# Optimization experiments

Measured on AMD Instinct MI355X. Metric: run time of the kernel, lower is better.

## Reference

```python
import jax, jax.numpy as jnp
import numpy as np

H = 128  # hidden/input size fixed by module


def setup_inputs() -> dict:
    key = jax.random.key(0)
    ks = jax.random.split(key, 8)
    S, B = 512, 256
    scale = 1.0 / np.sqrt(H)
    return {
        "X": jax.random.normal(ks[0], (S, B, H), dtype=jnp.float32),
        "h": jax.random.normal(ks[1], (1, B, H), dtype=jnp.float32),
        "lin_W": jax.random.uniform(ks[2], (H, H), jnp.float32, -scale, scale),
        "lin_b": jax.random.uniform(ks[3], (H,), jnp.float32, -scale, scale),
        "W_ih": jax.random.uniform(ks[4], (3 * H, H), jnp.float32, -scale, scale),
        "W_hh": jax.random.uniform(ks[5], (3 * H, H), jnp.float32, -scale, scale),
        "b_ih": jax.random.uniform(ks[6], (3 * H,), jnp.float32, -scale, scale),
        "b_hh": jax.random.uniform(ks[7], (3 * H,), jnp.float32, -scale, scale),
    }


def reference(X, h, lin_W, lin_b, W_ih, W_hh, b_ih, b_hh):
    # Linear: y = X @ W^T + b   (torch nn.Linear convention)
    Xp = jnp.einsum("sbd,ed->sbe", X, lin_W) + lin_b
    # Precompute input-hidden gate projections for all timesteps: (S, B, 3H)
    gx_all = jnp.einsum("sbd,gd->sbg", Xp, W_ih) + b_ih

    def step(h_t, gx):
        gh = h_t @ W_hh.T + b_hh  # (B, 3H)
        xr, xz, xn = jnp.split(gx, 3, axis=-1)
        hr, hz, hn = jnp.split(gh, 3, axis=-1)
        r = jax.nn.sigmoid(xr + hr)
        z = jax.nn.sigmoid(xz + hz)
        n = jnp.tanh(xn + r * hn)
        h_new = (1.0 - z) * n + z * h_t
        return h_new, h_new

    _, outs = jax.lax.scan(step, h[0], gx_all)
    return outs  # (S, B, H) — the module returns only the output sequence
```

## Files before the change

### kernel.cpp

```cpp
#include <hip/hip_runtime.h>
#include <math.h>

#define HID 128
#define G3  384
#define BATCH 256
#define SEQ 512
#define NB 16
#define NBLK (BATCH/NB)
#define NB2 2
#define NBLK2 (BATCH/NB2)
#define GHP 392

typedef __bf16 bf16x8 __attribute__((ext_vector_type(8)));
typedef __bf16 bf16x4 __attribute__((ext_vector_type(4)));
typedef float  f32x4  __attribute__((ext_vector_type(4)));

#define LOG2E 1.44269504088896f
#define SC_RZ (-1.44269504088896f)
#define SC_N  (-2.88539008177793f)

__device__ __forceinline__ float sigm(float x) {
    return __builtin_amdgcn_rcpf(1.f + __builtin_amdgcn_exp2f(-LOG2E * x));
}
__device__ __forceinline__ float tanh_fast(float x) {
    float e = __builtin_amdgcn_exp2f(-2.f * LOG2E * x);
    return __builtin_amdgcn_rcpf(1.f + e) * 2.f - 1.f;
}
__device__ __forceinline__ f32x4 mfma16(bf16x8 a, bf16x8 b, f32x4 c) {
    return __builtin_amdgcn_mfma_f32_16x16x32_bf16(a, b, c, 0, 0, 0);
}
__device__ __forceinline__ bf16x8 cvt8(float4 a, float4 b) {
    bf16x8 f;
    f[0] = (__bf16)a.x; f[1] = (__bf16)a.y; f[2] = (__bf16)a.z; f[3] = (__bf16)a.w;
    f[4] = (__bf16)b.x; f[5] = (__bf16)b.y; f[6] = (__bf16)b.z; f[7] = (__bf16)b.w;
    return f;
}
__device__ __forceinline__ bf16x8 cvt8s(float4 a, float4 b, float s) {
    bf16x8 f;
    f[0] = (__bf16)(a.x*s); f[1] = (__bf16)(a.y*s); f[2] = (__bf16)(a.z*s); f[3] = (__bf16)(a.w*s);
    f[4] = (__bf16)(b.x*s); f[5] = (__bf16)(b.y*s); f[6] = (__bf16)(b.z*s); f[7] = (__bf16)(b.w*s);
    return f;
}
__device__ __forceinline__ bf16x4 cvt4(float4 a) {
    bf16x4 f;
    f[0] = (__bf16)a.x; f[1] = (__bf16)a.y; f[2] = (__bf16)a.z; f[3] = (__bf16)a.w;
    return f;
}


__global__ void fold_bf16_kernel(const float* __restrict__ lin_W,
                                 const float* __restrict__ lin_b,
                                 const float* __restrict__ W_ih,
                                 const float* __restrict__ b_ih,
                                 __bf16* __restrict__ Wcbf,
                                 float* __restrict__ bcA) {
    const int g = blockIdx.x;
    const int d = threadIdx.x;
    const float sc = (g < 2 * HID) ? SC_RZ : SC_N;
    float acc = 0.f;
    #pragma unroll 16
    for (int e = 0; e < HID; ++e) acc += W_ih[g * HID + e] * lin_W[e * HID + d];
    Wcbf[g * HID + d] = (__bf16)(acc * sc);
    if (d == 0) {
        float b = 0.f;
        for (int e = 0; e < HID; ++e) b += W_ih[g * HID + e] * lin_b[e];
        bcA[g] = (b + b_ih[g]) * sc;
    }
}

#define GEMM_TILE(MT, CUR, NXT)                                               \
  {                                                                           \
    int mtn_ = (MT) + 1; if (mtn_ > 7) mtn_ = 7;                              \
    const float* pxn_ = X + (size_t)(m0 + mtn_ * 16 + col) * HID + lr * 8;    \
    _Pragma("unroll")                                                         \
    for (int kt = 0; kt < 4; ++kt) {                                          \
        NXT[2 * kt]     = *(const float4*)(pxn_ + kt * 32);                   \
        NXT[2 * kt + 1] = *(const float4*)(pxn_ + kt * 32 + 4);               \
    }                                                                         \
    bf16x8 Bx_[4];                                                            \
    _Pragma("unroll")                                                         \
    for (int kt = 0; kt < 4; ++kt) Bx_[kt] = cvt8(CUR[2 * kt], CUR[2 * kt + 1]); \
    const int m_ = m0 + (MT) * 16 + col;                                      \
    _Pragma("unroll")                                                         \
    for (int j = 0; j < 6; ++j) {                                             \
        f32x4 acc_ = vb[j];                                                   \
        acc_ = mfma16(A[j][0], Bx_[0], acc_);                                 \
        acc_ = mfma16(A[j][1], Bx_[1], acc_);                                 \
        acc_ = mfma16(A[j][2], Bx_[2], acc_);                                 \
        acc_ = mfma16(A[j][3], Bx_[3], acc_);                                 \
        float4 o_; o_.x = acc_[0]; o_.y = acc_[1]; o_.z = acc_[2]; o_.w = acc_[3]; \
        *(bf16x4*)(gx + (size_t)m_ * G3 + (w * 6 + j) * 16 + lr * 4) = cvt4(o_); \
    }                                                                         \
  }

__global__ __launch_bounds__(256, 2)
void gemm_gx2(const float* __restrict__ X,
              const __bf16* __restrict__ Wcbf,
              const float* __restrict__ bcA,
              __bf16* __restrict__ gx) {
    const int t   = threadIdx.x;
    const int w   = t >> 6;
    const int l   = t & 63;
    const int col = l & 15;
    const int lr  = l >> 4;
    const int m0  = blockIdx.x * 128;

    bf16x8 A[6][4];
    #pragma unroll
    for (int j = 0; j < 6; ++j)
        #pragma unroll
        for (int kt = 0; kt < 4; ++kt)
            A[j][kt] = *(const bf16x8*)(Wcbf +
                (size_t)((w * 6 + j) * 16 + col) * HID + kt * 32 + lr * 8);
    #pragma unroll
    for (int j = 0; j < 6; ++j)
        #pragma unroll
        for (int kt = 0; kt < 4; ++kt)
            asm volatile("" : "+v"(A[j][kt]));

    f32x4 vb[6];
    #pragma unroll
    for (int j = 0; j < 6; ++j)
        vb[j] = *(const f32x4*)(bcA + (w * 6 + j) * 16 + lr * 4);

    float4 xe[8], xo[8];
    {
        const float* px = X + (size_t)(m0 + col) * HID + lr * 8;
        #pragma unroll
        for (int kt = 0; kt < 4; ++kt) {
            xe[2 * kt]     = *(const float4*)(px + kt * 32);
            xe[2 * kt + 1] = *(const float4*)(px + kt * 32 + 4);
        }
    }
    for (int mt = 0; mt < 8; mt += 2) {
        GEMM_TILE(mt,     xe, xo);
        GEMM_TILE(mt + 1, xo, xe);
    }
}

#define SPLIT_STEP(S, C0, C1, C2, N0, N1, N2)                                 \
  {                                                                           \
               \
    bf16x8 Bh_[4];                                                            \
    _Pragma("unroll")                                                         \
    for (int kt = 0; kt < 4; ++kt)                                            \
        Bh_[kt] = *(const bf16x8*)(hbuf + SW(col, kt * 64 + lr * 16));        \
    f32x4 ar_ = vbr, az_ = vbz, anh_ = vbnh;                                  \
    _Pragma("unroll")                                                         \
    for (int kt = 0; kt < 4; ++kt) {                                          \
        ar_  = mfma16(aW[0][kt], Bh_[kt], ar_);                               \
        az_  = mfma16(aW[1][kt], Bh_[kt], az_);                               \
        anh_ = mfma16(aW[2][kt], Bh_[kt], anh_);                              \
    }                                                                         \
    if (col < NB2) {                                                          \
        float* gp_ = ghsF + col * GHP + w * 16 + lr * 4;                      \
        *(f32x4*)(gp_)       = ar_;                                           \
        *(f32x4*)(gp_ + 128) = az_;                                           \
        *(f32x4*)(gp_ + 256) = anh_;                                          \
    }                                                                         \
    asm volatile("s_waitcnt lgkmcnt(0)" ::: "memory");                        \
    __builtin_amdgcn_s_barrier();                                             \
                           \
    if (t < 256) {                                                            \
        int sp_ = (S) + 1; if (sp_ > SEQ - 1) sp_ = SEQ - 1;                  \
        const __bf16* p_ = gx + (size_t)sp_ * (BATCH * G3) + gxoff;           \
        asm volatile("global_load_ushort %0, %3, off\n\t"                     \
                     "global_load_ushort %1, %3, off offset:256\n\t"          \
                     "global_load_ushort %2, %3, off offset:512"              \
                     : "=&v"(N0), "=&v"(N1), "=&v"(N2) : "v"(p_) : "memory"); \
        float gr_ = ghsF[bi * GHP + ri];                                      \
        float gz_ = ghsF[bi * GHP + 128 + ri];                                \
        float gn_ = ghsF[bi * GHP + 256 + ri];                                \
          \
        asm volatile("s_waitcnt vmcnt(4)" ::: "memory");                      \
        __builtin_amdgcn_sched_barrier(0);                                    \
        float xr_ = __uint_as_float((C0) << 16);                              \
        float xz_ = __uint_as_float((C1) << 16);                              \
        float xn_ = __uint_as_float((C2) << 16);                              \
        float r_ = __builtin_amdgcn_rcpf(1.f + __builtin_amdgcn_exp2f(gr_ + xr_)); \
        float z_ = __builtin_amdgcn_rcpf(1.f + __builtin_amdgcn_exp2f(gz_ + xz_)); \
        float n_ = 2.f * __builtin_amdgcn_rcpf(1.f + __builtin_amdgcn_exp2f(xn_ + r_ * gn_)) - 1.f; \
        float hn_ = n_ + z_ * (hold - n_);                                    \
        hold = hn_;                                                           \
        *(__bf16*)(hbuf + SW(bi, ri * 2)) = (__bf16)hn_;                      \
        out[((size_t)(S) * BATCH + bb + bi) * HID + ri] = hn_;                \
    }                                                                         \
    asm volatile("s_waitcnt lgkmcnt(0)" ::: "memory");                        \
    __builtin_amdgcn_s_barrier();                                             \
  }

__global__ __launch_bounds__(512, 2)
void gru_scan_split2(const float* __restrict__ h0,
                     const float* __restrict__ W_hh,
                     const float* __restrict__ b_hh,
                     const __bf16* __restrict__ gx,
                     float* __restrict__ out) {
    const int t   = threadIdx.x;
    const int w   = t >> 6;
    const int l   = t & 63;
    const int col = l & 15;
    const int lr  = l >> 4;
    const int bb  = blockIdx.x * NB2;
    const int bi  = t >> 7;
    const int ri  = t & 127;

    __shared__ __align__(16) unsigned char lds[4096 + NB2 * GHP * 4];
    unsigned char* hbuf = lds;
    float* ghsF = (float*)(lds + 4096);

    auto SW = [](int b, int off) { return b * 256 + (off ^ ((b & 7) << 4)); };

    bf16x8 aW[3][4];
    #pragma unroll
    for (int g3 = 0; g3 < 3; ++g3) {
        const float s = (g3 < 2) ? SC_RZ : SC_N;
        #pragma unroll
        for (int kt = 0; kt < 4; ++kt) {
            const int row = g3 * HID + w * 16 + col;
            const float* pw = W_hh + row * HID + kt * 32 + lr * 8;
            aW[g3][kt] = cvt8s(*(const float4*)pw, *(const float4*)(pw + 4), s);
        }
    }
    #pragma unroll
    for (int g3 = 0; g3 < 3; ++g3)
        #pragma unroll
        for (int kt = 0; kt < 4; ++kt)
            asm volatile("" : "+v"(aW[g3][kt]));

    f32x4 vbr, vbz, vbnh;
    #pragma unroll
    for (int q = 0; q < 4; ++q) {
        const int g = w * 16 + lr * 4 + q;
        vbr[q]  = b_hh[g] * SC_RZ;
        vbz[q]  = b_hh[HID + g] * SC_RZ;
        vbnh[q] = b_hh[2 * HID + g] * SC_N;
    }

    float hold = 0.f;
    if (t < 256) hold = h0[(size_t)(bb + bi) * HID + ri];
    asm volatile("" :: "v"(hold), "v"(vbr), "v"(vbz), "v"(vbnh));

    const size_t gxoff = (size_t)(bb + bi) * G3 + ri;

    if (t < 32) {
        const int sb = t >> 4, k8 = (t & 15) * 8;
        const float* ph = h0 + (size_t)(bb + sb) * HID + k8;
        *(bf16x8*)(hbuf + SW(sb, k8 * 2)) =
            cvt8(*(const float4*)ph, *(const float4*)(ph + 4));
    } else if (t < 256) {
        const int sb = t >> 4, k8 = (t & 15) * 8;
        uint4 z = {0u, 0u, 0u, 0u};
        *(uint4*)(hbuf + SW(sb, k8 * 2)) = z;
    }

    unsigned c0 = 0, c1 = 0, c2 = 0, n0, n1, n2, dm;
    if (t < 256) {
        const __bf16* p_ = gx + gxoff;
        asm volatile("global_load_ushort %0, %3, off\n\t"
                     "global_load_ushort %1, %3, off offset:256\n\t"
                     "global_load_ushort %2, %3, off offset:512"
                     : "=&v"(c0), "=&v"(c1), "=&v"(c2) : "v"(p_) : "memory");
        asm volatile("global_load_ushort %0, %1, off"
                     : "=&v"(dm) : "v"(p_) : "memory");
    }
    asm volatile("s_waitcnt lgkmcnt(0)" ::: "memory");
    __builtin_amdgcn_s_barrier();

    for (int s0 = 0; s0 < SEQ; s0 += 2) {
        SPLIT_STEP(s0,     c0, c1, c2, n0, n1, n2);
        SPLIT_STEP(s0 + 1, n0, n1, n2, c0, c1, c2);
    }
    if (t < 256) asm volatile("" :: "v"(dm));
}

__global__ void fold_kernel(const float* __restrict__ lin_W,
                            const float* __restrict__ lin_b,
                            const float* __restrict__ W_ih,
                            const float* __restrict__ b_ih,
                            float* __restrict__ Wc,
                            float* __restrict__ bcA) {
    const int g = blockIdx.x;
    const int d = threadIdx.x;
    float acc = 0.f;
    for (int e = 0; e < HID; ++e) acc += W_ih[g * HID + e] * lin_W[e * HID + d];
    Wc[g * HID + d] = acc;
    if (d == 0) {
        float b = 0.f;
        for (int e = 0; e < HID; ++e) b += W_ih[g * HID + e] * lin_b[e];
        bcA[g] = b + b_ih[g];
    }
}

__global__ __launch_bounds__(512, 2)
void gru_scan_mfma(const float* __restrict__ X,
                   const float* __restrict__ h0,
                   const float* __restrict__ W_hh,
                   const float* __restrict__ b_hh,
                   const float* __restrict__ Wc,
                   const float* __restrict__ bcA,
                   float* __restrict__ out) {
    const int t   = threadIdx.x;
    const int w   = t >> 6;
    const int l   = t & 63;
    const int col = l & 15;
    const int lr  = l >> 4;
    const int bb  = blockIdx.x * NB;

    __shared__ __align__(16) unsigned char lds[16384];
    unsigned char* hA = lds;
    unsigned char* hB = lds + 4096;
    unsigned char* xA = lds + 8192;
    unsigned char* xB = lds + 12288;

    auto SW = [](int b, int off) { return b * 256 + (off ^ ((b & 7) << 4)); };

    bf16x8 aW[3][4], aC[3][4];
    #pragma unroll
    for (int g3 = 0; g3 < 3; ++g3)
        #pragma unroll
        for (int kt = 0; kt < 4; ++kt) {
            const int row = g3 * HID + w * 16 + col;
            const float* pw = W_hh + row * HID + kt * 32 + lr * 8;
            const float* pc = Wc   + row * HID + kt * 32 + lr * 8;
            aW[g3][kt] = cvt8(*(const float4*)pw, *(const float4*)(pw + 4));
            aC[g3][kt] = cvt8(*(const float4*)pc, *(const float4*)(pc + 4));
        }
    #pragma unroll
    for (int g3 = 0; g3 < 3; ++g3)
        #pragma unroll
        for (int kt = 0; kt < 4; ++kt) {
            asm volatile("" : "+v"(aW[g3][kt]));
            asm volatile("" : "+v"(aC[g3][kt]));
        }

    f32x4 vbr, vbz, vbnx, vbnh;
    #pragma unroll
    for (int q = 0; q < 4; ++q) {
        const int g = w * 16 + lr * 4 + q;
        vbr[q]  = bcA[g] + b_hh[g];
        vbz[q]  = bcA[HID + g] + b_hh[HID + g];
        vbnx[q] = bcA[2 * HID + g];
        vbnh[q] = b_hh[2 * HID + g];
    }

    f32x4 hold = *(const f32x4*)(h0 + (size_t)(bb + col) * HID + w * 16 + lr * 4);

    const int sb = t >> 5;
    const int sk = (t & 31) * 4;

    float4 xp, xq;
    if (t < 256) {
        const int hb = t >> 4, hk = (t & 15) * 8;
        const float* ph = h0 + (size_t)(bb + hb) * HID + hk;
        *(bf16x8*)(hA + SW(hb, hk * 2)) =
            cvt8(*(const float4*)ph, *(const float4*)(ph + 4));
    }
    {
        const float* px = X + ((size_t)0 * BATCH + bb + sb) * HID + sk;
        *(bf16x4*)(xA + SW(sb, sk * 2)) = cvt4(*(const float4*)px);
        const float* p1 = X + ((size_t)1 * BATCH + bb + sb) * HID + sk;
        xp = *(const float4*)p1;
    }
    asm volatile("s_waitcnt lgkmcnt(0)" ::: "memory");
    __builtin_amdgcn_s_barrier();

    auto STEP = [&](int s, unsigned char* hR, unsigned char* hW,
                    unsigned char* xR, unsigned char* xW,
                    float4& xc, float4& xn) {
        *(bf16x4*)(xW + SW(sb, sk * 2)) = cvt4(xc);
        {
            int sp = s + 2; if (sp > SEQ - 1) sp = SEQ - 1;
            const float* px = X + ((size_t)sp * BATCH + bb + sb) * HID + sk;
            xn = *(const float4*)px;
        }
        bf16x8 Bh[4], Bx[4];
        #pragma unroll
        for (int kt = 0; kt < 4; ++kt) {
            Bh[kt] = *(const bf16x8*)(hR + SW(col, kt * 64 + lr * 16));
            Bx[kt] = *(const bf16x8*)(xR + SW(col, kt * 64 + lr * 16));
        }
        f32x4 ar = vbr, az = vbz, anh = vbnh, anx = vbnx;
        #pragma unroll
        for (int kt = 0; kt < 4; ++kt) {
            ar  = mfma16(aW[0][kt], Bh[kt], ar);
            ar  = mfma16(aC[0][kt], Bx[kt], ar);
            az  = mfma16(aW[1][kt], Bh[kt], az);
            az  = mfma16(aC[1][kt], Bx[kt], az);
            anh = mfma16(aW[2][kt], Bh[kt], anh);
            anx = mfma16(aC[2][kt], Bx[kt], anx);
        }
        f32x4 hnew;
        #pragma unroll
        for (int q = 0; q < 4; ++q) {
            float r = sigm(ar[q]);
            float z = sigm(az[q]);
            float n = tanh_fast(anx[q] + r * anh[q]);
            hnew[q] = n + z * (hold[q] - n);
        }
        hold = hnew;
        *(bf16x4*)(hW + SW(col, (w * 16 + lr * 4) * 2)) = cvt4(*(float4*)&hnew);
        float4 o; o.x = hnew[0]; o.y = hnew[1]; o.z = hnew[2]; o.w = hnew[3];
        *(float4*)(out + ((size_t)s * BATCH + bb + col) * HID + w * 16 + lr * 4) = o;
        asm volatile("s_waitcnt lgkmcnt(0)" ::: "memory");
        __builtin_amdgcn_s_barrier();
    };

    for (int s0 = 0; s0 < SEQ; s0 += 2) {
        STEP(s0,     hA, hB, xA, xB, xp, xq);
        STEP(s0 + 1, hB, hA, xB, xA, xq, xp);
    }
}

extern "C" void kernel_launch(void* const* d_in, const int* in_sizes, int n_in,
                              void* d_out, int out_size, void* d_ws, size_t ws_size,
                              hipStream_t stream) {
    const float* X     = (const float*)d_in[0];
    const float* h0    = (const float*)d_in[1];
    const float* lin_W = (const float*)d_in[2];
    const float* lin_b = (const float*)d_in[3];
    const float* W_ih  = (const float*)d_in[4];
    const float* W_hh  = (const float*)d_in[5];
    const float* b_ih  = (const float*)d_in[6];
    const float* b_hh  = (const float*)d_in[7];
    float* out = (float*)d_out;

    const size_t GX_BYTES   = (size_t)SEQ * BATCH * G3 * 2;
    const size_t WCBF_BYTES = (size_t)G3 * HID * 2;
    const size_t BCA_BYTES  = (size_t)G3 * 4;

    if (ws_size >= GX_BYTES + WCBF_BYTES + BCA_BYTES) {
        __bf16* gxp  = (__bf16*)d_ws;
        __bf16* Wcbf = (__bf16*)((char*)d_ws + GX_BYTES);
        float*  bcA  = (float*)((char*)d_ws + GX_BYTES + WCBF_BYTES);

        fold_bf16_kernel<<<G3, HID, 0, stream>>>(lin_W, lin_b, W_ih, b_ih, Wcbf, bcA);
        gemm_gx2<<<(SEQ * BATCH) / 128, 256, 0, stream>>>(X, Wcbf, bcA, gxp);
        gru_scan_split2<<<NBLK2, 512, 0, stream>>>(h0, W_hh, b_hh, gxp, out);
    } else {
        float* Wc  = (float*)d_ws;
        float* bcA = Wc + G3 * HID;
        fold_kernel<<<G3, HID, 0, stream>>>(lin_W, lin_b, W_ih, b_ih, Wc, bcA);
        gru_scan_mfma<<<NBLK, 512, 0, stream>>>(X, h0, W_hh, b_hh, Wc, bcA, out);
    }
}
```

Before: 354.3 us.

## Fuse input-projection GEMM into scan kernel with per-timestep-group readiness counters

```diff
diff --git a/kernel.cpp b/kernel.cpp
--- a/kernel.cpp
+++ b/kernel.cpp
@@ -7,8 +7,9 @@
 #define SEQ 512
 #define NB 16
 #define NBLK (BATCH/NB)
-#define NB2 2
-#define NBLK2 (BATCH/NB2)
+#define NBS 2
+#define NBLKS (BATCH/NBS)
+#define NGEMM 1024
 #define GHP 392
 
 typedef __bf16 bf16x8 __attribute__((ext_vector_type(8)));
@@ -68,10 +69,11 @@
     }
 }
 
-#define GEMM_TILE(MT, CUR, NXT)                                               \
+
+#define GEMM_TILE4(MT, CUR, NXT)                                              \
   {                                                                           \
-    int mtn_ = (MT) + 1; if (mtn_ > 7) mtn_ = 7;                              \
-    const float* pxn_ = X + (size_t)(m0 + mtn_ * 16 + col) * HID + lr * 8;    \
+    int mtn_ = (MT) + 1; if (mtn_ > 3) mtn_ = 3;                              \
+    const float* pxn_ = X + (size_t)(m0h + mtn_ * 16 + col) * HID + lr * 8;   \
     _Pragma("unroll")                                                         \
     for (int kt = 0; kt < 4; ++kt) {                                          \
         NXT[2 * kt]     = *(const float4*)(pxn_ + kt * 32);                   \
@@ -80,7 +82,7 @@
     bf16x8 Bx_[4];                                                            \
     _Pragma("unroll")                                                         \
     for (int kt = 0; kt < 4; ++kt) Bx_[kt] = cvt8(CUR[2 * kt], CUR[2 * kt + 1]); \
-    const int m_ = m0 + (MT) * 16 + col;                                      \
+    const int m_ = m0h + (MT) * 16 + col;                                     \
     _Pragma("unroll")                                                         \
     for (int j = 0; j < 6; ++j) {                                             \
         f32x4 acc_ = vb[j];                                                   \
@@ -89,54 +91,9 @@
         acc_ = mfma16(A[j][2], Bx_[2], acc_);                                 \
         acc_ = mfma16(A[j][3], Bx_[3], acc_);                                 \
         float4 o_; o_.x = acc_[0]; o_.y = acc_[1]; o_.z = acc_[2]; o_.w = acc_[3]; \
-        *(bf16x4*)(gx + (size_t)m_ * G3 + (w * 6 + j) * 16 + lr * 4) = cvt4(o_); \
+        *(bf16x4*)(gx + (size_t)m_ * G3 + (w4 * 6 + j) * 16 + lr * 4) = cvt4(o_); \
     }                                                                         \
   }
-
-__global__ __launch_bounds__(256, 2)
-void gemm_gx2(const float* __restrict__ X,
-              const __bf16* __restrict__ Wcbf,
-              const float* __restrict__ bcA,
-              __bf16* __restrict__ gx) {
-    const int t   = threadIdx.x;
-    const int w   = t >> 6;
-    const int l   = t & 63;
-    const int col = l & 15;
-    const int lr  = l >> 4;
-    const int m0  = blockIdx.x * 128;
-
-    bf16x8 A[6][4];
-    #pragma unroll
-    for (int j = 0; j < 6; ++j)
-        #pragma unroll
-        for (int kt = 0; kt < 4; ++kt)
-            A[j][kt] = *(const bf16x8*)(Wcbf +
-                (size_t)((w * 6 + j) * 16 + col) * HID + kt * 32 + lr * 8);
-    #pragma unroll
-    for (int j = 0; j < 6; ++j)
-        #pragma unroll
-        for (int kt = 0; kt < 4; ++kt)
-            asm volatile("" : "+v"(A[j][kt]));
-
-    f32x4 vb[6];
-    #pragma unroll
-    for (int j = 0; j < 6; ++j)
-        vb[j] = *(const f32x4*)(bcA + (w * 6 + j) * 16 + lr * 4);
-
-    float4 xe[8], xo[8];
-    {
-        const float* px = X + (size_t)(m0 + col) * HID + lr * 8;
-        #pragma unroll
-        for (int kt = 0; kt < 4; ++kt) {
-            xe[2 * kt]     = *(const float4*)(px + kt * 32);
-            xe[2 * kt + 1] = *(const float4*)(px + kt * 32 + 4);
-        }
-    }
-    for (int mt = 0; mt < 8; mt += 2) {
-        GEMM_TILE(mt,     xe, xo);
-        GEMM_TILE(mt + 1, xo, xe);
-    }
-}
 
 #define SPLIT_STEP(S, C0, C1, C2, N0, N1, N2)                                 \
   {                                                                           \
@@ -152,7 +109,7 @@
         az_  = mfma16(aW[1][kt], Bh_[kt], az_);                               \
         anh_ = mfma16(aW[2][kt], Bh_[kt], anh_);                              \
     }                                                                         \
-    if (col < NB2) {                                                          \
+    if (col < NBS) {                                                          \
         float* gp_ = ghsF + col * GHP + w * 16 + lr * 4;                      \
         *(f32x4*)(gp_)       = ar_;                                           \
         *(f32x4*)(gp_ + 128) = az_;                                           \
@@ -163,6 +120,15 @@
                            \
     if (t < 256) {                                                            \
         int sp_ = (S) + 1; if (sp_ > SEQ - 1) sp_ = SEQ - 1;                  \
+                               \
+        int g_ = sp_ >> 3;                                                    \
+        if (g_ != curgrp) {                                                   \
+            curgrp = g_;                                                      \
+            while (__hip_atomic_load(cnt + g_, __ATOMIC_RELAXED,              \
+                                     __HIP_MEMORY_SCOPE_AGENT) < 16u)         \
+                __builtin_amdgcn_s_sleep(2);                                  \
+            __threadfence();                                                  \
+        }                                                                     \
         const __bf16* p_ = gx + (size_t)sp_ * (BATCH * G3) + gxoff;           \
         asm volatile("global_load_ushort %0, %3, off\n\t"                     \
                      "global_load_ushort %1, %3, off offset:256\n\t"          \
@@ -171,7 +137,6 @@
         float gr_ = ghsF[bi * GHP + ri];                                      \
         float gz_ = ghsF[bi * GHP + 128 + ri];                                \
         float gn_ = ghsF[bi * GHP + 256 + ri];                                \
-          \
         asm volatile("s_waitcnt vmcnt(4)" ::: "memory");                      \
         __builtin_amdgcn_sched_barrier(0);                                    \
         float xr_ = __uint_as_float((C0) << 16);                              \
@@ -190,21 +155,75 @@
   }
 
 __global__ __launch_bounds__(512, 2)
-void gru_scan_split2(const float* __restrict__ h0,
+void fused_gemm_scan(const float* __restrict__ X,
+                     const __bf16* __restrict__ Wcbf,
+                     const float* __restrict__ bcA,
+                     __bf16* __restrict__ gx,
+                     unsigned* __restrict__ cnt,
+                     const float* __restrict__ h0,
                      const float* __restrict__ W_hh,
                      const float* __restrict__ b_hh,
-                     const __bf16* __restrict__ gx,
                      float* __restrict__ out) {
-    const int t   = threadIdx.x;
+    const int t = threadIdx.x;
+
+    if (blockIdx.x >= NBLKS) {
+        const int chunk = blockIdx.x - NBLKS;
+        const int wg  = t >> 8;
+        const int w4  = (t >> 6) & 3;
+        const int l   = t & 63;
+        const int col = l & 15;
+        const int lr  = l >> 4;
+        const int m0h = chunk * 128 + wg * 64;
+
+        bf16x8 A[6][4];
+        #pragma unroll
+        for (int j = 0; j < 6; ++j)
+            #pragma unroll
+            for (int kt = 0; kt < 4; ++kt)
+                A[j][kt] = *(const bf16x8*)(Wcbf +
+                    (size_t)((w4 * 6 + j) * 16 + col) * HID + kt * 32 + lr * 8);
+        #pragma unroll
+        for (int j = 0; j < 6; ++j)
+            #pragma unroll
+            for (int kt = 0; kt < 4; ++kt)
+                asm volatile("" : "+v"(A[j][kt]));
+
+        f32x4 vb[6];
+        #pragma unroll
+        for (int j = 0; j < 6; ++j)
+            vb[j] = *(const f32x4*)(bcA + (w4 * 6 + j) * 16 + lr * 4);
+
+        float4 xe[8], xo[8];
+        {
+            const float* px = X + (size_t)(m0h + col) * HID + lr * 8;
+            #pragma unroll
+            for (int kt = 0; kt < 4; ++kt) {
+                xe[2 * kt]     = *(const float4*)(px + kt * 32);
+                xe[2 * kt + 1] = *(const float4*)(px + kt * 32 + 4);
+            }
+        }
+        GEMM_TILE4(0, xe, xo);
+        GEMM_TILE4(1, xo, xe);
+        GEMM_TILE4(2, xe, xo);
+        GEMM_TILE4(3, xo, xe);
+
+        __syncthreads();
+        if (t == 0) {
+            __threadfence();
+            atomicAdd(&cnt[chunk >> 4], 1u);
+        }
+        return;
+    }
+
     const int w   = t >> 6;
     const int l   = t & 63;
     const int col = l & 15;
     const int lr  = l >> 4;
-    const int bb  = blockIdx.x * NB2;
+    const int bb  = blockIdx.x * NBS;
     const int bi  = t >> 7;
     const int ri  = t & 127;
 
-    __shared__ __align__(16) unsigned char lds[4096 + NB2 * GHP * 4];
+    __shared__ __align__(16) unsigned char lds[4096 + NBS * GHP * 4];
     unsigned char* hbuf = lds;
     float* ghsF = (float*)(lds + 4096);
 
@@ -253,8 +272,13 @@
         *(uint4*)(hbuf + SW(sb, k8 * 2)) = z;
     }
 
+    int curgrp = 0;
     unsigned c0 = 0, c1 = 0, c2 = 0, n0, n1, n2, dm;
     if (t < 256) {
+        while (__hip_atomic_load(cnt + 0, __ATOMIC_RELAXED,
+                                 __HIP_MEMORY_SCOPE_AGENT) < 16u)
+            __builtin_amdgcn_s_sleep(8);
+        __threadfence();
         const __bf16* p_ = gx + gxoff;
         asm volatile("global_load_ushort %0, %3, off\n\t"
                      "global_load_ushort %1, %3, off offset:256\n\t"
@@ -427,15 +451,18 @@
     const size_t GX_BYTES   = (size_t)SEQ * BATCH * G3 * 2;
     const size_t WCBF_BYTES = (size_t)G3 * HID * 2;
     const size_t BCA_BYTES  = (size_t)G3 * 4;
-
-    if (ws_size >= GX_BYTES + WCBF_BYTES + BCA_BYTES) {
-        __bf16* gxp  = (__bf16*)d_ws;
-        __bf16* Wcbf = (__bf16*)((char*)d_ws + GX_BYTES);
-        float*  bcA  = (float*)((char*)d_ws + GX_BYTES + WCBF_BYTES);
-
+    const size_t CNT_BYTES  = 64 * sizeof(unsigned);
+
+    if (ws_size >= GX_BYTES + WCBF_BYTES + BCA_BYTES + CNT_BYTES) {
+        __bf16*   gxp  = (__bf16*)d_ws;
+        __bf16*   Wcbf = (__bf16*)((char*)d_ws + GX_BYTES);
+        float*    bcA  = (float*)((char*)d_ws + GX_BYTES + WCBF_BYTES);
+        unsigned* cnt  = (unsigned*)((char*)d_ws + GX_BYTES + WCBF_BYTES + BCA_BYTES);
+
+        hipMemsetAsync(cnt, 0, CNT_BYTES, stream);
         fold_bf16_kernel<<<G3, HID, 0, stream>>>(lin_W, lin_b, W_ih, b_ih, Wcbf, bcA);
-        gemm_gx2<<<(SEQ * BATCH) / 128, 256, 0, stream>>>(X, Wcbf, bcA, gxp);
-        gru_scan_split2<<<NBLK2, 512, 0, stream>>>(h0, W_hh, b_hh, gxp, out);
+        fused_gemm_scan<<<NBLKS + NGEMM, 512, 0, stream>>>(
+            X, Wcbf, bcA, gxp, cnt, h0, W_hh, b_hh, out);
     } else {
         float* Wc  = (float*)d_ws;
         float* bcA = Wc + G3 * HID;
```

After: 1.077 ms. 3.04x slower.
